# Optimization experiments

Hardware: AMD Instinct MI355X
Metric: run time of the kernel (lower is better)

The kernel has to match this reference:

```python
import jax, jax.numpy as jnp
import numpy as np
from jax import lax

C = 128
HEADS = 4
HEAD_DIM = C // HEADS
SCALE = HEAD_DIM ** (-0.5)


def conv2d(x, w, b, pad):
    # x: (B, Cin, H, W), w: (Cout, Cin, kh, kw)
    y = lax.conv_general_dilated(
        x, w, window_strides=(1, 1), padding=[(pad, pad), (pad, pad)],
        dimension_numbers=("NCHW", "OIHW", "NCHW"))
    return y + b[None, :, None, None]


def setup_inputs() -> dict:
    key = jax.random.key(0)
    ks = jax.random.split(key, 16)
    B, H, W = 2, 64, 64
    fan_1x1 = 1.0 / np.sqrt(C)
    fan_3x3a = 1.0 / np.sqrt(1 * 9)
    fan_3x3b = 1.0 / np.sqrt((C // 4) * 9)
    inp = {
        "sr_feat": jax.random.normal(ks[0], (B, C, H, W), jnp.float32),
        "seg_mask": jax.random.uniform(ks[1], (B, 1, H, W), jnp.float32),
        "Wq": jax.random.uniform(ks[2], (C, C, 1, 1), jnp.float32, -fan_1x1, fan_1x1),
        "bq": jnp.zeros((C,), jnp.float32),
        "Wm1": jax.random.uniform(ks[3], (C // 4, 1, 3, 3), jnp.float32, -fan_3x3a, fan_3x3a),
        "bm1": jnp.zeros((C // 4,), jnp.float32),
        "Wm2": jax.random.uniform(ks[4], (C, C // 4, 3, 3), jnp.float32, -fan_3x3b, fan_3x3b),
        "bm2": jnp.zeros((C,), jnp.float32),
        "Wk": jax.random.uniform(ks[5], (C, C, 1, 1), jnp.float32, -fan_1x1, fan_1x1),
        "bk": jnp.zeros((C,), jnp.float32),
        "Wv": jax.random.uniform(ks[6], (C, C, 1, 1), jnp.float32, -fan_1x1, fan_1x1),
        "bv": jnp.zeros((C,), jnp.float32),
        "Wo": jax.random.uniform(ks[7], (C, C, 1, 1), jnp.float32, -fan_1x1, fan_1x1),
        "bo": jnp.zeros((C,), jnp.float32),
    }
    return inp


def reference(sr_feat, seg_mask, Wq, bq, Wm1, bm1, Wm2, bm2, Wk, bk, Wv, bv, Wo, bo):
    B, Cc, H, W = sr_feat.shape
    # mask_embed: conv3x3 -> relu -> conv3x3 (seg_mask already at (H, W))
    mask_feat = conv2d(jax.nn.relu(conv2d(seg_mask, Wm1, bm1, 1)), Wm2, bm2, 1)
    q = conv2d(sr_feat, Wq, bq, 0)
    k = conv2d(mask_feat, Wk, bk, 0)
    v = conv2d(mask_feat, Wv, bv, 0)
    hw = H * W
    # (B, C, HW) -> (B, heads, HW, head_dim)
    def split_heads(t):
        return t.reshape(B, HEADS, HEAD_DIM, hw).transpose(0, 1, 3, 2)
    qh, kh, vh = split_heads(q), split_heads(k), split_heads(v)
    attn = jnp.einsum("bhqd,bhkd->bhqk", qh, kh) * SCALE
    attn = jax.nn.softmax(attn, axis=-1)
    guided = jnp.einsum("bhqk,bhkd->bhqd", attn, vh)  # (B, heads, HW, head_dim)
    guided = guided.transpose(0, 1, 3, 2).reshape(B, Cc, H, W)
    return conv2d(guided, Wo, bo, 0) + sr_feat
```

## Files before the change

### kernel.cpp

```cpp
#include <hip/hip_runtime.h>
#include <hip/hip_bf16.h>

#define HW 4096
#define CC 128
#define SCALE_LOG2E (0.17677669529663687f * 1.4426950408889634f)
#define KSPLIT 8
#define H1PAD 4096

typedef short bf16x8 __attribute__((ext_vector_type(8)));
typedef float f32x4 __attribute__((ext_vector_type(4)));

static __device__ __forceinline__ unsigned short f2bf(float f) {
  unsigned int u = __float_as_uint(f);
  unsigned int r = (u + 0x7fffu + ((u >> 16) & 1u)) >> 16;
  return (unsigned short)r;
}
static __device__ __forceinline__ unsigned int pk2bf(float lo, float hi) {
  return __builtin_amdgcn_perm(__float_as_uint(hi), __float_as_uint(lo),
                               0x07060302u);
}
static __device__ __forceinline__ unsigned int pk2bf_rne(float lo, float hi) {
  return (unsigned int)f2bf(lo) | ((unsigned int)f2bf(hi) << 16);
}
static __device__ __forceinline__ f32x4 mfma16(bf16x8 a, bf16x8 b, f32x4 c) {
  return __builtin_amdgcn_mfma_f32_16x16x32_bf16(a, b, c, 0, 0, 0);
}

__global__ __launch_bounds__(256) void prep_kernel(
    const float* __restrict__ Wq, const float* __restrict__ Wk,
    const float* __restrict__ Wv, const float* __restrict__ Wo,
    const float* __restrict__ Wm2, const float* __restrict__ seg,
    const float* __restrict__ Wm1, const float* __restrict__ bm1,
    unsigned short* __restrict__ wbf, unsigned short* __restrict__ wm2t,
    unsigned short* __restrict__ h1p) {
  __shared__ float wls[288];
  const int blk = blockIdx.x;
  const int t = threadIdx.x;
  if (blk < 256) {
    int i = blk * 256 + t;
    int which = i >> 14, j = i & 16383;
    const float* src = which == 0 ? Wq : which == 1 ? Wk : which == 2 ? Wv : Wo;
    float v = src[j];
    if (which == 0) v *= SCALE_LOG2E;
    wbf[i] = f2bf(v);
  } else if (blk < 400) {
    int i = (blk - 256) * 256 + t;
    int tap = i >> 12;
    int rem = i & 4095;
    int co = rem >> 5, ci = rem & 31;
    wm2t[i] = f2bf(Wm2[co * 288 + ci * 9 + tap]);
  } else {
    for (int j = t; j < 288; j += 256) wls[j] = Wm1[j];
    const int idx = (blk - 400) * 256 + t;
    const int b = idx >> 12, p = idx & 4095;
    const int x = p & 63, y = p >> 6;
    const float* sb = seg + b * HW;
    float pix[9];
#pragma unroll
    for (int tap = 0; tap < 9; ++tap) {
      int dy = tap / 3 - 1, dx = tap % 3 - 1;
      int xx = x + dx, yy = y + dy;
      bool valid = ((unsigned)xx < 64u) & ((unsigned)yy < 64u);
      pix[tap] = valid ? sb[yy * 64 + xx] : 0.f;
    }
    __syncthreads();
    unsigned int pk[16];
#pragma unroll
    for (int cg = 0; cg < 16; ++cg) {
      float s0 = bm1[2 * cg], s1 = bm1[2 * cg + 1];
#pragma unroll
      for (int tap = 0; tap < 9; ++tap) {
        s0 += wls[(2 * cg) * 9 + tap] * pix[tap];
        s1 += wls[(2 * cg + 1) * 9 + tap] * pix[tap];
      }
      pk[cg] = pk2bf_rne(fmaxf(s0, 0.f), fmaxf(s1, 0.f));
    }
    unsigned short* dst = h1p + (size_t)idx * 32;
#pragma unroll
    for (int g = 0; g < 4; ++g) *(uint4*)(dst + g * 8) = *(uint4*)&pk[g * 4];
  }
}

__global__ __launch_bounds__(256) void conv2qkv_mfma(
    const float* __restrict__ sr, const unsigned short* __restrict__ h1p,
    const unsigned short* __restrict__ wm2t, const float* __restrict__ bm2,
    const unsigned short* __restrict__ wq, const float* __restrict__ bq,
    const unsigned short* __restrict__ wk, const float* __restrict__ bk,
    const unsigned short* __restrict__ wv, const float* __restrict__ bv,
    unsigned short* __restrict__ qt, unsigned short* __restrict__ kt,
    unsigned short* __restrict__ vt) {
  const int b   = blockIdx.y;
  const int px0 = blockIdx.x * 32;
  const int t   = threadIdx.x;
  const int w = t >> 6, lane = t & 63, col = lane & 15, quad = lane >> 4;

  __shared__ unsigned short mT[32][136];
  __shared__ unsigned short xT[32][136];

  for (int r = 0; r < 16; ++r) {
    int idx = r * 256 + t;
    int ci = idx >> 5, px = idx & 31;
    xT[px][ci] = f2bf(sr[((size_t)b * CC + ci) * HW + px0 + px]);
  }

  {
    bf16x8 afrag[9][2];
#pragma unroll
    for (int tap = 0; tap < 9; ++tap) {
      const unsigned short* wb =
          wm2t + ((size_t)tap * 128 + w * 32 + col) * 32 + quad * 8;
      afrag[tap][0] = *(const bf16x8*)wb;
      afrag[tap][1] = *(const bf16x8*)(wb + 16 * 32);
    }
    const unsigned short* xb = h1p + (size_t)b * HW * 32;
    f32x4 acc[2][2] = {};
    const bf16x8 zf = {0, 0, 0, 0, 0, 0, 0, 0};
    const int px[2] = {px0 + col, px0 + 16 + col};
    const int xx[2] = {px[0] & 63, px[1] & 63};
    const int yy[2] = {px[0] >> 6, px[1] >> 6};
#pragma unroll
    for (int tap = 0; tap < 9; ++tap) {
      const int dy = tap / 3 - 1, dx = tap % 3 - 1;
      const int shift = dy * 64 + dx;
#pragma unroll
      for (int pt = 0; pt < 2; ++pt) {
        bool valid =
            ((unsigned)(xx[pt] + dx) < 64u) & ((unsigned)(yy[pt] + dy) < 64u);
        bf16x8 bf = *(const bf16x8*)(xb + (size_t)(px[pt] + shift) * 32 + quad * 8);
        bf = valid ? bf : zf;
        acc[0][pt] = mfma16(afrag[tap][0], bf, acc[0][pt]);
        acc[1][pt] = mfma16(afrag[tap][1], bf, acc[1][pt]);
      }
    }
#pragma unroll
    for (int ct = 0; ct < 2; ++ct) {
      float4 bb = *(const float4*)(bm2 + w * 32 + ct * 16 + quad * 4);
#pragma unroll
      for (int pt = 0; pt < 2; ++pt) {
        uint2 pk = {pk2bf_rne(acc[ct][pt][0] + bb.x, acc[ct][pt][1] + bb.y),
                    pk2bf_rne(acc[ct][pt][2] + bb.z, acc[ct][pt][3] + bb.w)};
        *(uint2*)&mT[pt * 16 + col][w * 32 + ct * 16 + quad * 4] = pk;
      }
    }
  }
  __syncthreads();

  f32x4 aq[2][2] = {}, ak[2][2] = {}, av[2][2] = {};
  const unsigned short* wqb = wq + (size_t)(w * 32 + col) * CC + quad * 8;
  const unsigned short* wkb = wk + (size_t)(w * 32 + col) * CC + quad * 8;
  const unsigned short* wvb = wv + (size_t)(w * 32 + col) * CC + quad * 8;
#pragma unroll
  for (int ks = 0; ks < 4; ++ks) {
    bf16x8 qa0 = *(const bf16x8*)(wqb + ks * 32);
    bf16x8 qa1 = *(const bf16x8*)(wqb + 16 * CC + ks * 32);
    bf16x8 ka0 = *(const bf16x8*)(wkb + ks * 32);
    bf16x8 ka1 = *(const bf16x8*)(wkb + 16 * CC + ks * 32);
    bf16x8 va0 = *(const bf16x8*)(wvb + ks * 32);
    bf16x8 va1 = *(const bf16x8*)(wvb + 16 * CC + ks * 32);
    bf16x8 bx0 = *(const bf16x8*)&xT[col][ks * 32 + quad * 8];
    bf16x8 bx1 = *(const bf16x8*)&xT[16 + col][ks * 32 + quad * 8];
    bf16x8 bm0 = *(const bf16x8*)&mT[col][ks * 32 + quad * 8];
    bf16x8 bm1f = *(const bf16x8*)&mT[16 + col][ks * 32 + quad * 8];
    aq[0][0] = mfma16(qa0, bx0, aq[0][0]);
    aq[0][1] = mfma16(qa0, bx1, aq[0][1]);
    aq[1][0] = mfma16(qa1, bx0, aq[1][0]);
    aq[1][1] = mfma16(qa1, bx1, aq[1][1]);
    ak[0][0] = mfma16(ka0, bm0, ak[0][0]);
    ak[0][1] = mfma16(ka0, bm1f, ak[0][1]);
    ak[1][0] = mfma16(ka1, bm0, ak[1][0]);
    ak[1][1] = mfma16(ka1, bm1f, ak[1][1]);
    av[0][0] = mfma16(va0, bm0, av[0][0]);
    av[0][1] = mfma16(va0, bm1f, av[0][1]);
    av[1][0] = mfma16(va1, bm0, av[1][0]);
    av[1][1] = mfma16(va1, bm1f, av[1][1]);
  }
  const int bh = b * 4 + w;
  const int chunk = blockIdx.x;
#pragma unroll
  for (int ct = 0; ct < 2; ++ct) {
    float4 bbq = *(const float4*)(bq + w * 32 + ct * 16 + quad * 4);
    float4 bbk = *(const float4*)(bk + w * 32 + ct * 16 + quad * 4);
    float4 bbv = *(const float4*)(bv + w * 32 + ct * 16 + quad * 4);
#pragma unroll
    for (int pt = 0; pt < 2; ++pt) {
      int key = pt * 16 + col;
      uint2 pkq = {pk2bf_rne(aq[ct][pt][0] + bbq.x * SCALE_LOG2E,
                             aq[ct][pt][1] + bbq.y * SCALE_LOG2E),
                   pk2bf_rne(aq[ct][pt][2] + bbq.z * SCALE_LOG2E,
                             aq[ct][pt][3] + bbq.w * SCALE_LOG2E)};
      *(uint2*)(qt + ((size_t)bh * HW + px0 + key) * 32 + ct * 16 + quad * 4) = pkq;
      uint2 pkk = {pk2bf_rne(ak[ct][pt][0] + bbk.x, ak[ct][pt][1] + bbk.y),
                   pk2bf_rne(ak[ct][pt][2] + bbk.z, ak[ct][pt][3] + bbk.w)};
      *(uint2*)(kt + ((size_t)bh * HW + px0 + key) * 32 + ct * 16 + quad * 4) = pkk;
      unsigned short* vdst =
          vt + (((size_t)bh * 128 + chunk) * 32 + ct * 16 + quad * 4) * 32 + key;
      vdst[0]  = f2bf(av[ct][pt][0] + bbv.x);
      vdst[32] = f2bf(av[ct][pt][1] + bbv.y);
      vdst[64] = f2bf(av[ct][pt][2] + bbv.z);
      vdst[96] = f2bf(av[ct][pt][3] + bbv.w);
    }
  }
}

__global__ __launch_bounds__(256, 4) void attn_mfma_kernel(
    const unsigned short* __restrict__ qt, const unsigned short* __restrict__ ktg,
    const unsigned short* __restrict__ vt, unsigned short* __restrict__ opart,
    float* __restrict__ lpart) {
  const int bh   = blockIdx.y;
  const int s    = blockIdx.z;
  const int t    = threadIdx.x;
  const int wave = t >> 6;
  const int lane = t & 63;
  const int col  = lane & 15;
  const int quad = lane >> 4;
  const int q0w  = blockIdx.x * 256 + wave * 64;

  const unsigned short* Qb = qt  + (size_t)bh * HW * 32;
  const unsigned short* Kb = ktg + (size_t)bh * HW * 32;
  const unsigned short* Vc = vt  + (size_t)bh * 128 * 1024;

  __shared__ unsigned short Pt[4][4][16][40];

  bf16x8 qf[4];
#pragma unroll
  for (int qt_i = 0; qt_i < 4; ++qt_i)
    qf[qt_i] = *(const bf16x8*)(Qb + (size_t)(q0w + qt_i * 16 + col) * 32 + quad * 8);

  float lacc[4] = {0.f, 0.f, 0.f, 0.f};
  f32x4 o[4][2] = {};
  const f32x4 zero = {0.f, 0.f, 0.f, 0.f};

  const unsigned short* kp1 = Kb + (size_t)(s * 16) * 1024 + col * 32 + quad * 8;
  const unsigned short* kp2 = kp1 + 512;
  const unsigned short* vp1 = Vc + (size_t)(s * 16) * 1024 + col * 32 + quad * 8;
  const unsigned short* vp2 = vp1 + 512;

  bf16x8 kf1 = *(const bf16x8*)(kp1);
  bf16x8 kf2 = *(const bf16x8*)(kp2);
  bf16x8 vf1 = *(const bf16x8*)(vp1);
  bf16x8 vf2 = *(const bf16x8*)(vp2);

  for (int c = 0; c < 16; ++c) {
    bf16x8 nk1 = *(const bf16x8*)(kp1 + (c + 1) * 1024);
    bf16x8 nk2 = *(const bf16x8*)(kp2 + (c + 1) * 1024);
    bf16x8 nv1 = *(const bf16x8*)(vp1 + (c + 1) * 1024);
    bf16x8 nv2 = *(const bf16x8*)(vp2 + (c + 1) * 1024);
#pragma unroll
    for (int qt_i = 0; qt_i < 4; ++qt_i) {
      f32x4 s1 = mfma16(kf1, qf[qt_i], zero);
      f32x4 s2 = mfma16(kf2, qf[qt_i], zero);
      float p0 = __builtin_amdgcn_exp2f(s1[0]);
      float p1 = __builtin_amdgcn_exp2f(s1[1]);
      float p2 = __builtin_amdgcn_exp2f(s1[2]);
      float p3 = __builtin_amdgcn_exp2f(s1[3]);
      float p4 = __builtin_amdgcn_exp2f(s2[0]);
      float p5 = __builtin_amdgcn_exp2f(s2[1]);
      float p6 = __builtin_amdgcn_exp2f(s2[2]);
      float p7 = __builtin_amdgcn_exp2f(s2[3]);
      lacc[qt_i] += ((p0 + p1) + (p2 + p3)) + ((p4 + p5) + (p6 + p7));

      uint2 w1 = {pk2bf(p0, p1), pk2bf(p2, p3)};
      uint2 w2 = {pk2bf(p4, p5), pk2bf(p6, p7)};
      *(uint2*)&Pt[wave][qt_i][col][quad * 4]      = w1;
      *(uint2*)&Pt[wave][qt_i][col][16 + quad * 4] = w2;
      bf16x8 pf = *(const bf16x8*)&Pt[wave][qt_i][col][quad * 8];

      o[qt_i][0] = mfma16(vf1, pf, o[qt_i][0]);
      o[qt_i][1] = mfma16(vf2, pf, o[qt_i][1]);
    }
    kf1 = nk1; kf2 = nk2; vf1 = nv1; vf2 = nv2;
  }

#pragma unroll
  for (int qt_i = 0; qt_i < 4; ++qt_i) {
    float l = lacc[qt_i];
    l += __shfl_xor(l, 16);
    l += __shfl_xor(l, 32);
    int qq = q0w + qt_i * 16 + col;
    size_t base = ((size_t)(s * 8 + bh) * HW + qq) * 32;
    uint2 w1 = {pk2bf_rne(o[qt_i][0][0], o[qt_i][0][1]),
                pk2bf_rne(o[qt_i][0][2], o[qt_i][0][3])};
    uint2 w2 = {pk2bf_rne(o[qt_i][1][0], o[qt_i][1][1]),
                pk2bf_rne(o[qt_i][1][2], o[qt_i][1][3])};
    *(uint2*)(opart + base + quad * 4)      = w1;
    *(uint2*)(opart + base + 16 + quad * 4) = w2;
    if (quad == 0) lpart[(size_t)(s * 8 + bh) * HW + qq] = l;
  }
}

__global__ __launch_bounds__(256) void combine_convo(
    const unsigned short* __restrict__ opart, const float* __restrict__ lpart,
    const unsigned short* __restrict__ wo, const float* __restrict__ bo,
    const float* __restrict__ sr, float* __restrict__ out) {
  const int b   = blockIdx.y;
  const int px0 = blockIdx.x * 32;
  const int t   = threadIdx.x;

  __shared__ unsigned short gT[32][136];

  {
    const int px = t & 31, cs = t >> 5;
    const int q  = px0 + px;
    const int bh = b * 4 + (cs >> 1);
    const int d0 = (cs & 1) * 16;
    float lsum = 0.f;
#pragma unroll
    for (int s = 0; s < KSPLIT; ++s) lsum += lpart[(size_t)(s * 8 + bh) * HW + q];
    float inv = 1.f / lsum;
    float acc[16];
#pragma unroll
    for (int j = 0; j < 16; ++j) acc[j] = 0.f;
#pragma unroll
    for (int s = 0; s < KSPLIT; ++s) {
      const unsigned short* src =
          opart + ((size_t)(s * 8 + bh) * HW + q) * 32 + d0;
#pragma unroll
      for (int g = 0; g < 2; ++g) {
        uint4 raw = *(const uint4*)(src + g * 8);
        const unsigned int* u = (const unsigned int*)&raw;
#pragma unroll
        for (int h = 0; h < 4; ++h) {
          acc[g * 8 + 2 * h]     += __uint_as_float(u[h] << 16);
          acc[g * 8 + 2 * h + 1] += __uint_as_float(u[h] & 0xffff0000u);
        }
      }
    }
    unsigned int pk[8];
#pragma unroll
    for (int j = 0; j < 8; ++j)
      pk[j] = pk2bf_rne(acc[2 * j] * inv, acc[2 * j + 1] * inv);
    *(uint4*)&gT[px][cs * 16]     = *(uint4*)&pk[0];
    *(uint4*)&gT[px][cs * 16 + 8] = *(uint4*)&pk[4];
  }
  __syncthreads();

  const int w = t >> 6, lane = t & 63, col = lane & 15, quad = lane >> 4;
  f32x4 acc2[2][2] = {};
  const unsigned short* wbase = wo + (size_t)(w * 32 + col) * CC + quad * 8;
#pragma unroll
  for (int ks = 0; ks < 4; ++ks) {
    bf16x8 a0 = *(const bf16x8*)(wbase + ks * 32);
    bf16x8 a1 = *(const bf16x8*)(wbase + 16 * CC + ks * 32);
    bf16x8 b0 = *(const bf16x8*)&gT[col][ks * 32 + quad * 8];
    bf16x8 b1 = *(const bf16x8*)&gT[16 + col][ks * 32 + quad * 8];
    acc2[0][0] = mfma16(a0, b0, acc2[0][0]);
    acc2[0][1] = mfma16(a0, b1, acc2[0][1]);
    acc2[1][0] = mfma16(a1, b0, acc2[1][0]);
    acc2[1][1] = mfma16(a1, b1, acc2[1][1]);
  }
#pragma unroll
  for (int ct = 0; ct < 2; ++ct) {
    float4 bb = *(const float4*)(bo + w * 32 + ct * 16 + quad * 4);
    float bias[4] = {bb.x, bb.y, bb.z, bb.w};
#pragma unroll
    for (int pt = 0; pt < 2; ++pt) {
      int px = px0 + pt * 16 + col;
      int co = w * 32 + ct * 16 + quad * 4;
      const float* rb = sr + ((size_t)b * CC + co) * HW + px;
      float* ob = out + ((size_t)b * CC + co) * HW + px;
#pragma unroll
      for (int r = 0; r < 4; ++r)
        ob[(size_t)r * HW] = acc2[ct][pt][r] + bias[r] + rb[(size_t)r * HW];
    }
  }
}

extern "C" void kernel_launch(void* const* d_in, const int* in_sizes, int n_in,
                              void* d_out, int out_size, void* d_ws, size_t ws_size,
                              hipStream_t stream) {
  const float* sr  = (const float*)d_in[0];
  const float* seg = (const float*)d_in[1];
  const float* Wq  = (const float*)d_in[2];
  const float* bq  = (const float*)d_in[3];
  const float* Wm1 = (const float*)d_in[4];
  const float* bm1 = (const float*)d_in[5];
  const float* Wm2 = (const float*)d_in[6];
  const float* bm2 = (const float*)d_in[7];
  const float* Wk  = (const float*)d_in[8];
  const float* bk  = (const float*)d_in[9];
  const float* Wv  = (const float*)d_in[10];
  const float* bv  = (const float*)d_in[11];
  const float* Wo  = (const float*)d_in[12];
  const float* bo  = (const float*)d_in[13];
  float* out = (float*)d_out;

  unsigned short* h1T = (unsigned short*)d_ws;
  unsigned short* h1p = h1T + H1PAD;
  unsigned short* qt  = h1T + H1PAD + 262144 + H1PAD;
  unsigned short* kt  = qt + 1048576;
  unsigned short* vt  = kt + 1048576;
  unsigned short* wbf = vt + 1048576;
  unsigned short* wm2t = wbf + 65536;
  unsigned short* opart = wm2t + 36864;
  float* lpart = (float*)(opart + (size_t)KSPLIT * 8 * HW * 32);

  const unsigned short* wq = wbf;
  const unsigned short* wk = wbf + 16384;
  const unsigned short* wv = wbf + 32768;
  const unsigned short* wo = wbf + 49152;

  prep_kernel<<<432, 256, 0, stream>>>(Wq, Wk, Wv, Wo, Wm2, seg, Wm1, bm1,
                                       wbf, wm2t, h1p);
  conv2qkv_mfma<<<dim3(128, 2), 256, 0, stream>>>(
      sr, h1p, wm2t, bm2, wq, bq, wk, bk, wv, bv, qt, kt, vt);
  attn_mfma_kernel<<<dim3(16, 8, KSPLIT), 256, 0, stream>>>(qt, kt, vt, opart,
                                                            lpart);
  combine_convo<<<dim3(128, 2), 256, 0, stream>>>(opart, lpart, wo, bo, sr, out);
}
```

Before: 130.6 us.

## Feed P from registers via 16x16x16 MFMA and halve conv tile width

The attention kernel no longer writes the exponentiated scores P to shared memory and reads them back in B-operand layout. It keeps each lane's four P values in registers and uses the K=16 bf16 MFMA variant twice per output tile, with V loaded as four 4-element fragments. Separately, the conv/QKV projection kernel now processes 16 pixels per block instead of 32, launching twice as many blocks for more parallelism. In exchange, the attention loop issues twice as many smaller MFMAs, and the conv kernel reloads the weight fragments once per 16 pixels instead of per 32.

After: 132.1 us. About the same (+1.2%).

```diff
diff --git a/kernel.cpp b/kernel.cpp
--- a/kernel.cpp
+++ b/kernel.cpp
@@ -8,6 +8,7 @@
 #define H1PAD 4096
 
 typedef short bf16x8 __attribute__((ext_vector_type(8)));
+typedef short bf16x4 __attribute__((ext_vector_type(4)));
 typedef float f32x4 __attribute__((ext_vector_type(4)));
 
 static __device__ __forceinline__ unsigned short f2bf(float f) {
@@ -24,6 +25,13 @@
 }
 static __device__ __forceinline__ f32x4 mfma16(bf16x8 a, bf16x8 b, f32x4 c) {
   return __builtin_amdgcn_mfma_f32_16x16x32_bf16(a, b, c, 0, 0, 0);
+}
+static __device__ __forceinline__ f32x4 mfma16k16(bf16x4 a, bf16x4 b, f32x4 c) {
+  return __builtin_amdgcn_mfma_f32_16x16x16bf16_1k(a, b, c, 0, 0, 0);
+}
+static __device__ __forceinline__ bf16x4 mkbf4(unsigned int lo, unsigned int hi) {
+  uint2 u = {lo, hi};
+  return *(bf16x4*)&u;
 }
 
 __global__ __launch_bounds__(256) void prep_kernel(
@@ -90,16 +98,16 @@
     unsigned short* __restrict__ qt, unsigned short* __restrict__ kt,
     unsigned short* __restrict__ vt) {
   const int b   = blockIdx.y;
-  const int px0 = blockIdx.x * 32;
+  const int px0 = blockIdx.x * 16;
   const int t   = threadIdx.x;
   const int w = t >> 6, lane = t & 63, col = lane & 15, quad = lane >> 4;
 
-  __shared__ unsigned short mT[32][136];
-  __shared__ unsigned short xT[32][136];
-
-  for (int r = 0; r < 16; ++r) {
+  __shared__ unsigned short mT[16][136];
+  __shared__ unsigned short xT[16][136];
+
+  for (int r = 0; r < 8; ++r) {
     int idx = r * 256 + t;
-    int ci = idx >> 5, px = idx & 31;
+    int ci = idx >> 4, px = idx & 15;
     xT[px][ci] = f2bf(sr[((size_t)b * CC + ci) * HW + px0 + px]);
   }
 
@@ -113,39 +121,31 @@
       afrag[tap][1] = *(const bf16x8*)(wb + 16 * 32);
     }
     const unsigned short* xb = h1p + (size_t)b * HW * 32;
-    f32x4 acc[2][2] = {};
+    f32x4 acc[2] = {};
     const bf16x8 zf = {0, 0, 0, 0, 0, 0, 0, 0};
-    const int px[2] = {px0 + col, px0 + 16 + col};
-    const int xx[2] = {px[0] & 63, px[1] & 63};
-    const int yy[2] = {px[0] >> 6, px[1] >> 6};
+    const int px = px0 + col;
+    const int xx = px & 63, yy = px >> 6;
 #pragma unroll
     for (int tap = 0; tap < 9; ++tap) {
       const int dy = tap / 3 - 1, dx = tap % 3 - 1;
       const int shift = dy * 64 + dx;
-#pragma unroll
-      for (int pt = 0; pt < 2; ++pt) {
-        bool valid =
-            ((unsigned)(xx[pt] + dx) < 64u) & ((unsigned)(yy[pt] + dy) < 64u);
-        bf16x8 bf = *(const bf16x8*)(xb + (size_t)(px[pt] + shift) * 32 + quad * 8);
-        bf = valid ? bf : zf;
-        acc[0][pt] = mfma16(afrag[tap][0], bf, acc[0][pt]);
-        acc[1][pt] = mfma16(afrag[tap][1], bf, acc[1][pt]);
-      }
+      bool valid = ((unsigned)(xx + dx) < 64u) & ((unsigned)(yy + dy) < 64u);
+      bf16x8 bf = *(const bf16x8*)(xb + (size_t)(px + shift) * 32 + quad * 8);
+      bf = valid ? bf : zf;
+      acc[0] = mfma16(afrag[tap][0], bf, acc[0]);
+      acc[1] = mfma16(afrag[tap][1], bf, acc[1]);
     }
 #pragma unroll
     for (int ct = 0; ct < 2; ++ct) {
       float4 bb = *(const float4*)(bm2 + w * 32 + ct * 16 + quad * 4);
-#pragma unroll
-      for (int pt = 0; pt < 2; ++pt) {
-        uint2 pk = {pk2bf_rne(acc[ct][pt][0] + bb.x, acc[ct][pt][1] + bb.y),
-                    pk2bf_rne(acc[ct][pt][2] + bb.z, acc[ct][pt][3] + bb.w)};
-        *(uint2*)&mT[pt * 16 + col][w * 32 + ct * 16 + quad * 4] = pk;
-      }
+      uint2 pk = {pk2bf_rne(acc[ct][0] + bb.x, acc[ct][1] + bb.y),
+                  pk2bf_rne(acc[ct][2] + bb.z, acc[ct][3] + bb.w)};
+      *(uint2*)&mT[col][w * 32 + ct * 16 + quad * 4] = pk;
     }
   }
   __syncthreads();
 
-  f32x4 aq[2][2] = {}, ak[2][2] = {}, av[2][2] = {};
+  f32x4 aq[2] = {}, ak[2] = {}, av[2] = {};
   const unsigned short* wqb = wq + (size_t)(w * 32 + col) * CC + quad * 8;
   const unsigned short* wkb = wk + (size_t)(w * 32 + col) * CC + quad * 8;
   const unsigned short* wvb = wv + (size_t)(w * 32 + col) * CC + quad * 8;
@@ -158,47 +158,37 @@
     bf16x8 va0 = *(const bf16x8*)(wvb + ks * 32);
     bf16x8 va1 = *(const bf16x8*)(wvb + 16 * CC + ks * 32);
     bf16x8 bx0 = *(const bf16x8*)&xT[col][ks * 32 + quad * 8];
-    bf16x8 bx1 = *(const bf16x8*)&xT[16 + col][ks * 32 + quad * 8];
     bf16x8 bm0 = *(const bf16x8*)&mT[col][ks * 32 + quad * 8];
-    bf16x8 bm1f = *(const bf16x8*)&mT[16 + col][ks * 32 + quad * 8];
-    aq[0][0] = mfma16(qa0, bx0, aq[0][0]);
-    aq[0][1] = mfma16(qa0, bx1, aq[0][1]);
-    aq[1][0] = mfma16(qa1, bx0, aq[1][0]);
-    aq[1][1] = mfma16(qa1, bx1, aq[1][1]);
-    ak[0][0] = mfma16(ka0, bm0, ak[0][0]);
-    ak[0][1] = mfma16(ka0, bm1f, ak[0][1]);
-    ak[1][0] = mfma16(ka1, bm0, ak[1][0]);
-    ak[1][1] = mfma16(ka1, bm1f, ak[1][1]);
-    av[0][0] = mfma16(va0, bm0, av[0][0]);
-    av[0][1] = mfma16(va0, bm1f, av[0][1]);
-    av[1][0] = mfma16(va1, bm0, av[1][0]);
-    av[1][1] = mfma16(va1, bm1f, av[1][1]);
+    aq[0] = mfma16(qa0, bx0, aq[0]);
+    aq[1] = mfma16(qa1, bx0, aq[1]);
+    ak[0] = mfma16(ka0, bm0, ak[0]);
+    ak[1] = mfma16(ka1, bm0, ak[1]);
+    av[0] = mfma16(va0, bm0, av[0]);
+    av[1] = mfma16(va1, bm0, av[1]);
   }
   const int bh = b * 4 + w;
-  const int chunk = blockIdx.x;
+  const int chunk = px0 >> 5;
+  const int keybase = px0 & 31;
 #pragma unroll
   for (int ct = 0; ct < 2; ++ct) {
     float4 bbq = *(const float4*)(bq + w * 32 + ct * 16 + quad * 4);
     float4 bbk = *(const float4*)(bk + w * 32 + ct * 16 + quad * 4);
     float4 bbv = *(const float4*)(bv + w * 32 + ct * 16 + quad * 4);
-#pragma unroll
-    for (int pt = 0; pt < 2; ++pt) {
-      int key = pt * 16 + col;
-      uint2 pkq = {pk2bf_rne(aq[ct][pt][0] + bbq.x * SCALE_LOG2E,
-                             aq[ct][pt][1] + bbq.y * SCALE_LOG2E),
-                   pk2bf_rne(aq[ct][pt][2] + bbq.z * SCALE_LOG2E,
-                             aq[ct][pt][3] + bbq.w * SCALE_LOG2E)};
-      *(uint2*)(qt + ((size_t)bh * HW + px0 + key) * 32 + ct * 16 + quad * 4) = pkq;
-      uint2 pkk = {pk2bf_rne(ak[ct][pt][0] + bbk.x, ak[ct][pt][1] + bbk.y),
-                   pk2bf_rne(ak[ct][pt][2] + bbk.z, ak[ct][pt][3] + bbk.w)};
-      *(uint2*)(kt + ((size_t)bh * HW + px0 + key) * 32 + ct * 16 + quad * 4) = pkk;
-      unsigned short* vdst =
-          vt + (((size_t)bh * 128 + chunk) * 32 + ct * 16 + quad * 4) * 32 + key;
-      vdst[0]  = f2bf(av[ct][pt][0] + bbv.x);
-      vdst[32] = f2bf(av[ct][pt][1] + bbv.y);
-      vdst[64] = f2bf(av[ct][pt][2] + bbv.z);
-      vdst[96] = f2bf(av[ct][pt][3] + bbv.w);
-    }
+    uint2 pkq = {pk2bf_rne(aq[ct][0] + bbq.x * SCALE_LOG2E,
+                           aq[ct][1] + bbq.y * SCALE_LOG2E),
+                 pk2bf_rne(aq[ct][2] + bbq.z * SCALE_LOG2E,
+                           aq[ct][3] + bbq.w * SCALE_LOG2E)};
+    *(uint2*)(qt + ((size_t)bh * HW + px0 + col) * 32 + ct * 16 + quad * 4) = pkq;
+    uint2 pkk = {pk2bf_rne(ak[ct][0] + bbk.x, ak[ct][1] + bbk.y),
+                 pk2bf_rne(ak[ct][2] + bbk.z, ak[ct][3] + bbk.w)};
+    *(uint2*)(kt + ((size_t)bh * HW + px0 + col) * 32 + ct * 16 + quad * 4) = pkk;
+    unsigned short* vdst =
+        vt + (((size_t)bh * 128 + chunk) * 32 + ct * 16 + quad * 4) * 32 +
+        keybase + col;
+    vdst[0]  = f2bf(av[ct][0] + bbv.x);
+    vdst[32] = f2bf(av[ct][1] + bbv.y);
+    vdst[64] = f2bf(av[ct][2] + bbv.z);
+    vdst[96] = f2bf(av[ct][3] + bbv.w);
   }
 }
 
@@ -219,8 +209,6 @@
   const unsigned short* Kb = ktg + (size_t)bh * HW * 32;
   const unsigned short* Vc = vt  + (size_t)bh * 128 * 1024;
 
-  __shared__ unsigned short Pt[4][4][16][40];
-
   bf16x8 qf[4];
 #pragma unroll
   for (int qt_i = 0; qt_i < 4; ++qt_i)
@@ -232,19 +220,25 @@
 
   const unsigned short* kp1 = Kb + (size_t)(s * 16) * 1024 + col * 32 + quad * 8;
   const unsigned short* kp2 = kp1 + 512;
-  const unsigned short* vp1 = Vc + (size_t)(s * 16) * 1024 + col * 32 + quad * 8;
-  const unsigned short* vp2 = vp1 + 512;
+  const unsigned short* vpa = Vc + (size_t)(s * 16) * 1024 + col * 32 + quad * 4;
+  const unsigned short* vpb = vpa + 16;
+  const unsigned short* vpc = vpa + 16 * 32;
+  const unsigned short* vpd = vpc + 16;
 
   bf16x8 kf1 = *(const bf16x8*)(kp1);
   bf16x8 kf2 = *(const bf16x8*)(kp2);
-  bf16x8 vf1 = *(const bf16x8*)(vp1);
-  bf16x8 vf2 = *(const bf16x8*)(vp2);
+  bf16x4 vfa = *(const bf16x4*)(vpa);
+  bf16x4 vfb = *(const bf16x4*)(vpb);
+  bf16x4 vfc = *(const bf16x4*)(vpc);
+  bf16x4 vfd = *(const bf16x4*)(vpd);
 
   for (int c = 0; c < 16; ++c) {
     bf16x8 nk1 = *(const bf16x8*)(kp1 + (c + 1) * 1024);
     bf16x8 nk2 = *(const bf16x8*)(kp2 + (c + 1) * 1024);
-    bf16x8 nv1 = *(const bf16x8*)(vp1 + (c + 1) * 1024);
-    bf16x8 nv2 = *(const bf16x8*)(vp2 + (c + 1) * 1024);
+    bf16x4 nva = *(const bf16x4*)(vpa + (c + 1) * 1024);
+    bf16x4 nvb = *(const bf16x4*)(vpb + (c + 1) * 1024);
+    bf16x4 nvc = *(const bf16x4*)(vpc + (c + 1) * 1024);
+    bf16x4 nvd = *(const bf16x4*)(vpd + (c + 1) * 1024);
 #pragma unroll
     for (int qt_i = 0; qt_i < 4; ++qt_i) {
       f32x4 s1 = mfma16(kf1, qf[qt_i], zero);
@@ -259,16 +253,15 @@
       float p7 = __builtin_amdgcn_exp2f(s2[3]);
       lacc[qt_i] += ((p0 + p1) + (p2 + p3)) + ((p4 + p5) + (p6 + p7));
 
-      uint2 w1 = {pk2bf(p0, p1), pk2bf(p2, p3)};
-      uint2 w2 = {pk2bf(p4, p5), pk2bf(p6, p7)};
-      *(uint2*)&Pt[wave][qt_i][col][quad * 4]      = w1;
-      *(uint2*)&Pt[wave][qt_i][col][16 + quad * 4] = w2;
-      bf16x8 pf = *(const bf16x8*)&Pt[wave][qt_i][col][quad * 8];
-
-      o[qt_i][0] = mfma16(vf1, pf, o[qt_i][0]);
-      o[qt_i][1] = mfma16(vf2, pf, o[qt_i][1]);
-    }
-    kf1 = nk1; kf2 = nk2; vf1 = nv1; vf2 = nv2;
+      bf16x4 pf1 = mkbf4(pk2bf(p0, p1), pk2bf(p2, p3));
+      bf16x4 pf2 = mkbf4(pk2bf(p4, p5), pk2bf(p6, p7));
+      o[qt_i][0] = mfma16k16(vfa, pf1, o[qt_i][0]);
+      o[qt_i][0] = mfma16k16(vfb, pf2, o[qt_i][0]);
+      o[qt_i][1] = mfma16k16(vfc, pf1, o[qt_i][1]);
+      o[qt_i][1] = mfma16k16(vfd, pf2, o[qt_i][1]);
+    }
+    kf1 = nk1; kf2 = nk2;
+    vfa = nva; vfb = nvb; vfc = nvc; vfd = nvd;
   }
 
 #pragma unroll
@@ -401,7 +394,7 @@
 
   prep_kernel<<<432, 256, 0, stream>>>(Wq, Wk, Wv, Wo, Wm2, seg, Wm1, bm1,
                                        wbf, wm2t, h1p);
-  conv2qkv_mfma<<<dim3(128, 2), 256, 0, stream>>>(
+  conv2qkv_mfma<<<dim3(256, 2), 256, 0, stream>>>(
       sr, h1p, wm2t, bm2, wq, bq, wk, bk, wv, bv, qt, kt, vt);
   attn_mfma_kernel<<<dim3(16, 8, KSPLIT), 256, 0, stream>>>(qt, kt, vt, opart,
                                                             lpart);
```

## Feed softmax probabilities straight from registers into K16 MFMAs, doubling key split

Applied to the files above, without the earlier changes.

The attention PV product now uses 16x16x16 bf16 MFMAs whose input layout matches the score accumulator layout. The exponentiated probabilities are packed in registers and passed directly, so the per-tile LDS write and read-back transpose of P goes away. The key split factor rises from 8 to 16, which halves the keys per block and doubles the grid. That adds more partial outputs to write and combine, and it uses twice as many smaller MFMA instructions for PV.

Measured after the change: 137.0 us. 4.9% more time.

```diff
diff --git a/kernel.cpp b/kernel.cpp
--- a/kernel.cpp
+++ b/kernel.cpp
@@ -4,10 +4,11 @@
 #define HW 4096
 #define CC 128
 #define SCALE_LOG2E (0.17677669529663687f * 1.4426950408889634f)
-#define KSPLIT 8
+#define KSPLIT 16
 #define H1PAD 4096
 
 typedef short bf16x8 __attribute__((ext_vector_type(8)));
+typedef short bf16x4 __attribute__((ext_vector_type(4)));
 typedef float f32x4 __attribute__((ext_vector_type(4)));
 
 static __device__ __forceinline__ unsigned short f2bf(float f) {
@@ -24,6 +25,13 @@
 }
 static __device__ __forceinline__ f32x4 mfma16(bf16x8 a, bf16x8 b, f32x4 c) {
   return __builtin_amdgcn_mfma_f32_16x16x32_bf16(a, b, c, 0, 0, 0);
+}
+static __device__ __forceinline__ f32x4 mfma16k16(bf16x4 a, bf16x4 b, f32x4 c) {
+  return __builtin_amdgcn_mfma_f32_16x16x16bf16_1k(a, b, c, 0, 0, 0);
+}
+static __device__ __forceinline__ bf16x4 mkbf4(unsigned int lo, unsigned int hi) {
+  uint2 u = {lo, hi};
+  return *(bf16x4*)&u;
 }
 
 __global__ __launch_bounds__(256) void prep_kernel(
@@ -219,8 +227,6 @@
   const unsigned short* Kb = ktg + (size_t)bh * HW * 32;
   const unsigned short* Vc = vt  + (size_t)bh * 128 * 1024;
 
-  __shared__ unsigned short Pt[4][4][16][40];
-
   bf16x8 qf[4];
 #pragma unroll
   for (int qt_i = 0; qt_i < 4; ++qt_i)
@@ -230,21 +236,27 @@
   f32x4 o[4][2] = {};
   const f32x4 zero = {0.f, 0.f, 0.f, 0.f};
 
-  const unsigned short* kp1 = Kb + (size_t)(s * 16) * 1024 + col * 32 + quad * 8;
+  const unsigned short* kp1 = Kb + (size_t)(s * 8) * 1024 + col * 32 + quad * 8;
   const unsigned short* kp2 = kp1 + 512;
-  const unsigned short* vp1 = Vc + (size_t)(s * 16) * 1024 + col * 32 + quad * 8;
-  const unsigned short* vp2 = vp1 + 512;
+  const unsigned short* vpa = Vc + (size_t)(s * 8) * 1024 + col * 32 + quad * 4;
+  const unsigned short* vpb = vpa + 16;
+  const unsigned short* vpc = vpa + 16 * 32;
+  const unsigned short* vpd = vpc + 16;
 
   bf16x8 kf1 = *(const bf16x8*)(kp1);
   bf16x8 kf2 = *(const bf16x8*)(kp2);
-  bf16x8 vf1 = *(const bf16x8*)(vp1);
-  bf16x8 vf2 = *(const bf16x8*)(vp2);
-
-  for (int c = 0; c < 16; ++c) {
+  bf16x4 vfa = *(const bf16x4*)(vpa);
+  bf16x4 vfb = *(const bf16x4*)(vpb);
+  bf16x4 vfc = *(const bf16x4*)(vpc);
+  bf16x4 vfd = *(const bf16x4*)(vpd);
+
+  for (int c = 0; c < 8; ++c) {
     bf16x8 nk1 = *(const bf16x8*)(kp1 + (c + 1) * 1024);
     bf16x8 nk2 = *(const bf16x8*)(kp2 + (c + 1) * 1024);
-    bf16x8 nv1 = *(const bf16x8*)(vp1 + (c + 1) * 1024);
-    bf16x8 nv2 = *(const bf16x8*)(vp2 + (c + 1) * 1024);
+    bf16x4 nva = *(const bf16x4*)(vpa + (c + 1) * 1024);
+    bf16x4 nvb = *(const bf16x4*)(vpb + (c + 1) * 1024);
+    bf16x4 nvc = *(const bf16x4*)(vpc + (c + 1) * 1024);
+    bf16x4 nvd = *(const bf16x4*)(vpd + (c + 1) * 1024);
 #pragma unroll
     for (int qt_i = 0; qt_i < 4; ++qt_i) {
       f32x4 s1 = mfma16(kf1, qf[qt_i], zero);
@@ -259,16 +271,15 @@
       float p7 = __builtin_amdgcn_exp2f(s2[3]);
       lacc[qt_i] += ((p0 + p1) + (p2 + p3)) + ((p4 + p5) + (p6 + p7));
 
-      uint2 w1 = {pk2bf(p0, p1), pk2bf(p2, p3)};
-      uint2 w2 = {pk2bf(p4, p5), pk2bf(p6, p7)};
-      *(uint2*)&Pt[wave][qt_i][col][quad * 4]      = w1;
-      *(uint2*)&Pt[wave][qt_i][col][16 + quad * 4] = w2;
-      bf16x8 pf = *(const bf16x8*)&Pt[wave][qt_i][col][quad * 8];
-
-      o[qt_i][0] = mfma16(vf1, pf, o[qt_i][0]);
-      o[qt_i][1] = mfma16(vf2, pf, o[qt_i][1]);
-    }
-    kf1 = nk1; kf2 = nk2; vf1 = nv1; vf2 = nv2;
+      bf16x4 pf1 = mkbf4(pk2bf(p0, p1), pk2bf(p2, p3));
+      bf16x4 pf2 = mkbf4(pk2bf(p4, p5), pk2bf(p6, p7));
+      o[qt_i][0] = mfma16k16(vfa, pf1, o[qt_i][0]);
+      o[qt_i][0] = mfma16k16(vfb, pf2, o[qt_i][0]);
+      o[qt_i][1] = mfma16k16(vfc, pf1, o[qt_i][1]);
+      o[qt_i][1] = mfma16k16(vfd, pf2, o[qt_i][1]);
+    }
+    kf1 = nk1; kf2 = nk2;
+    vfa = nva; vfb = nvb; vfc = nvc; vfd = nvd;
   }
 
 #pragma unroll
```
